# Kernel tuning notes

Hardware: AMD Instinct MI355X
Metric: run time of the kernel (lower is better)

## Reference

```python
import jax, jax.numpy as jnp
import numpy as np

N_NODES = 100000
N_EDGES = 1600000
IN_F = 256
OUT_F = 128


def setup_inputs() -> dict:
    key = jax.random.key(0)
    k1, k2, k3, k4, k5, k6 = jax.random.split(key, 6)
    init_range = float(np.sqrt(6.0 / (IN_F + OUT_F)))
    stdv = 1.0 / float(np.sqrt(OUT_F))
    return {
        "x": jax.random.normal(k1, (N_NODES, IN_F), dtype=jnp.float32),
        "weight": jax.random.uniform(k2, (IN_F, OUT_F), dtype=jnp.float32, minval=-init_range, maxval=init_range),
        "bias": jax.random.uniform(k3, (OUT_F,), dtype=jnp.float32, minval=-stdv, maxval=stdv),
        "adj_val": jax.random.uniform(k4, (N_EDGES,), dtype=jnp.float32),
        "adj_row": jax.random.randint(k5, (N_EDGES,), 0, N_NODES),  # destination node per edge
        "adj_col": jax.random.randint(k6, (N_EDGES,), 0, N_NODES),  # source node per edge
    }


def reference(x, weight, bias, adj_val, adj_row, adj_col):
    # support = X @ W   (dense GEMM, [N, in] x [in, out])
    support = x @ weight
    # output = spmm(adj, support): gather source rows, scale by edge value,
    # segment-sum into destination rows. Honors COO sparsity; no [N,N] dense.
    gathered = support[adj_col] * adj_val[:, None]          # [E, out]
    out = jax.ops.segment_sum(gathered, adj_row, num_segments=N_NODES)
    return out + bias
```

## Files before the change

kernel.cpp:

```cpp
#include <hip/hip_runtime.h>

#define N_NODES 100000
#define N_EDGES 1600000
#define IN_F 256
#define OUT_F 128
#define LDK 40

#define NBUCK 391
#define NCHUNK 256
#define CHUNK_E (N_EDGES / NCHUNK)
#define NSCAN (NBUCK * NCHUNK)
#define SCAN_BLK 4096
#define NSCAN_BLOCKS ((NSCAN + SCAN_BLK - 1) / SCAN_BLK)

#define GEMM_BM 64
#define GEMM_BLOCKS ((N_NODES + GEMM_BM - 1) / GEMM_BM)

typedef __attribute__((ext_vector_type(8))) short bf16x8;
typedef __attribute__((ext_vector_type(4))) float f32x4;

__device__ __forceinline__ unsigned short f2bf(float f) {
    unsigned u = __float_as_uint(f);
    unsigned r = u + 0x7fffu + ((u >> 16) & 1u);
    return (unsigned short)(r >> 16);
}

__global__ __launch_bounds__(256) void count_wtrans_kernel(const int* __restrict__ rowi,
                                                           int* __restrict__ counts,
                                                           const float* __restrict__ w,
                                                           unsigned short* __restrict__ wt) {
    const int tid = threadIdx.x;
    if (blockIdx.x >= NCHUNK) {
        int c = blockIdx.x - NCHUNK;
        wt[c * IN_F + tid] = f2bf(w[tid * OUT_F + c]);
        return;
    }
    __shared__ int hist[NBUCK];
    const int c = blockIdx.x;
    for (int i = tid; i < NBUCK; i += 256) hist[i] = 0;
    __syncthreads();
    const int e0 = c * CHUNK_E;
    for (int i = tid; i < CHUNK_E; i += 256)
        atomicAdd(&hist[rowi[e0 + i] >> 8], 1);
    __syncthreads();
    for (int i = tid; i < NBUCK; i += 256) counts[i * NCHUNK + c] = hist[i];
}

__global__ __launch_bounds__(256) void scan1_kernel(int* __restrict__ data,
                                                    int* __restrict__ blocksums,
                                                    int n) {
    __shared__ int sdata[256];
    const int tid = threadIdx.x;
    const int base = blockIdx.x * SCAN_BLK + tid * 16;
    int v[16];
    if (base < n) {
#pragma unroll
        for (int q = 0; q < 4; ++q) {
            int4 t = *reinterpret_cast<const int4*>(&data[base + q * 4]);
            v[q * 4 + 0] = t.x; v[q * 4 + 1] = t.y; v[q * 4 + 2] = t.z; v[q * 4 + 3] = t.w;
        }
    } else {
#pragma unroll
        for (int i = 0; i < 16; ++i) v[i] = 0;
    }
    int pre[16], run = 0;
#pragma unroll
    for (int i = 0; i < 16; ++i) { pre[i] = run; run += v[i]; }
    sdata[tid] = run;
    __syncthreads();
#pragma unroll
    for (int off = 1; off < 256; off <<= 1) {
        int t = (tid >= off) ? sdata[tid - off] : 0;
        __syncthreads();
        sdata[tid] += t;
        __syncthreads();
    }
    int excl = (tid == 0) ? 0 : sdata[tid - 1];
    if (base < n) {
#pragma unroll
        for (int q = 0; q < 4; ++q) {
            int4 t = {excl + pre[q * 4 + 0], excl + pre[q * 4 + 1],
                      excl + pre[q * 4 + 2], excl + pre[q * 4 + 3]};
            *reinterpret_cast<int4*>(&data[base + q * 4]) = t;
        }
    }
    if (tid == 255) blocksums[blockIdx.x] = sdata[255];
}

__global__ __launch_bounds__(256) void scan2_kernel(int* __restrict__ blocksums, int nblk) {
    __shared__ int sdata[256];
    const int tid = threadIdx.x;
    sdata[tid] = (tid < nblk) ? blocksums[tid] : 0;
    __syncthreads();
#pragma unroll
    for (int off = 1; off < 256; off <<= 1) {
        int t = (tid >= off) ? sdata[tid - off] : 0;
        __syncthreads();
        sdata[tid] += t;
        __syncthreads();
    }
    if (tid < nblk) blocksums[tid] = (tid == 0) ? 0 : sdata[tid - 1];
}

__global__ __launch_bounds__(256) void gemm_scatter_kernel(const float* __restrict__ x,
                                                           const unsigned short* __restrict__ wt,
                                                           unsigned short* __restrict__ support,
                                                           const int* __restrict__ rowi,
                                                           const int* __restrict__ coli,
                                                           const float* __restrict__ val,
                                                           const int* __restrict__ counts,
                                                           const int* __restrict__ blocksums,
                                                           uint2* __restrict__ tmp) {
    const int tid = threadIdx.x;

    if (blockIdx.x < NCHUNK) {
        __shared__ int cur[NBUCK];
        const int c = blockIdx.x;
        for (int i = tid; i < NBUCK; i += 256) {
            int j = i * NCHUNK + c;
            cur[i] = counts[j] + blocksums[j >> 12];
        }
        __syncthreads();
        const int e0 = c * CHUNK_E;
        for (int i = tid; i < CHUNK_E; i += 256) {
            int e = e0 + i;
            int dst = rowi[e];
            int b = dst >> 8;
            int pos = atomicAdd(&cur[b], 1);
            tmp[pos] = make_uint2(((unsigned)(dst & 255) << 17) | (unsigned)coli[e],
                                  __float_as_uint(val[e]));
        }
        return;
    }

    __shared__ unsigned short xs[GEMM_BM * LDK];
    __shared__ unsigned short ws[128 * LDK];

    const int lane = tid & 63;
    const int wv = tid >> 6;
    const int wr = (wv >> 1) * 32;
    const int wc = (wv & 1) * 64;
    const int row0 = (blockIdx.x - NCHUNK) * GEMM_BM;
    const int l15 = lane & 15;
    const int kg = (lane >> 4) * 8;

    f32x4 acc[2][4];
#pragma unroll
    for (int m = 0; m < 2; ++m)
#pragma unroll
        for (int n = 0; n < 4; ++n) acc[m][n] = (f32x4){0.f, 0.f, 0.f, 0.f};

    for (int kt = 0; kt < 8; ++kt) {
        __syncthreads();
#pragma unroll
        for (int i = 0; i < 2; ++i) {
            int idx = tid + 256 * i;
            int r = idx >> 3, q = idx & 7;
            int grow = row0 + r;
            if (grow > N_NODES - 1) grow = N_NODES - 1;
            float4 v = *reinterpret_cast<const float4*>(&x[(size_t)grow * IN_F + kt * 32 + q * 4]);
            ushort4 b;
            b.x = f2bf(v.x); b.y = f2bf(v.y); b.z = f2bf(v.z); b.w = f2bf(v.w);
            *reinterpret_cast<ushort4*>(&xs[r * LDK + q * 4]) = b;
        }
#pragma unroll
        for (int j = 0; j < 2; ++j) {
            int idx = tid + 256 * j;
            int c = idx >> 2, q = idx & 3;
            uint4 v = *reinterpret_cast<const uint4*>(&wt[c * IN_F + kt * 32 + q * 8]);
            *reinterpret_cast<uint4*>(&ws[c * LDK + q * 8]) = v;
        }
        __syncthreads();

        bf16x8 af[2], bfr[4];
#pragma unroll
        for (int m = 0; m < 2; ++m)
            af[m] = *reinterpret_cast<const bf16x8*>(&xs[(wr + m * 16 + l15) * LDK + kg]);
#pragma unroll
        for (int n = 0; n < 4; ++n)
            bfr[n] = *reinterpret_cast<const bf16x8*>(&ws[(wc + n * 16 + l15) * LDK + kg]);
#pragma unroll
        for (int m = 0; m < 2; ++m)
#pragma unroll
            for (int n = 0; n < 4; ++n)
                acc[m][n] = __builtin_amdgcn_mfma_f32_16x16x32_bf16(af[m], bfr[n], acc[m][n], 0, 0, 0);
    }

#pragma unroll
    for (int m = 0; m < 2; ++m) {
#pragma unroll
        for (int r = 0; r < 4; ++r) {
            int row = row0 + wr + m * 16 + (lane >> 4) * 4 + r;
            if (row < N_NODES) {
#pragma unroll
                for (int n = 0; n < 4; ++n) {
                    support[(size_t)row * OUT_F + wc + n * 16 + l15] = f2bf(acc[m][n][r]);
                }
            }
        }
    }
}

__global__ __launch_bounds__(256) void fine_kernel(const uint2* __restrict__ tmp,
                                                   const int* __restrict__ counts,
                                                   const int* __restrict__ blocksums,
                                                   uint2* __restrict__ pairs,
                                                   int* __restrict__ offsets) {
    __shared__ int hist[256];
    __shared__ int scanb[256];
    __shared__ int cur[256];
    const int tid = threadIdx.x, b = blockIdx.x;
    int j0 = b * NCHUNK;
    const int start = counts[j0] + blocksums[j0 >> 12];
    int end;
    if (b == NBUCK - 1) end = N_EDGES;
    else {
        int j1 = (b + 1) * NCHUNK;
        end = counts[j1] + blocksums[j1 >> 12];
    }

    hist[tid] = 0;
    __syncthreads();
    for (int i = start + tid; i < end; i += 256)
        atomicAdd(&hist[tmp[i].x >> 17], 1);
    __syncthreads();
    int h = hist[tid];
    scanb[tid] = h;
    __syncthreads();
#pragma unroll
    for (int off = 1; off < 256; off <<= 1) {
        int t = (tid >= off) ? scanb[tid - off] : 0;
        __syncthreads();
        scanb[tid] += t;
        __syncthreads();
    }
    cur[tid] = start + scanb[tid] - h;
    int node = (b << 8) + tid;
    if (node < N_NODES) offsets[node] = start + scanb[tid];
    __syncthreads();
    for (int i = start + tid; i < end; i += 256) {
        uint2 u = tmp[i];
        int dl = u.x >> 17;
        int pos = atomicAdd(&cur[dl], 1);
        pairs[pos] = make_uint2(u.x & 0x1FFFFu, u.y);
    }
}

__global__ __launch_bounds__(256) void accum_kernel(const unsigned short* __restrict__ support,
                                                    const uint2* __restrict__ pairs,
                                                    const int* __restrict__ offsets,
                                                    const float* __restrict__ bias,
                                                    float* __restrict__ out) {
    const int node = blockIdx.x * 4 + (threadIdx.x >> 6);
    const int lane = threadIdx.x & 63;
    const int grp = lane >> 4;
    const int l16 = lane & 15;
    if (node >= N_NODES) return;

    const int start = (node == 0) ? 0 : offsets[node - 1];
    const int end = offsets[node];

    float acc[8];
#pragma unroll
    for (int t = 0; t < 8; ++t) acc[t] = 0.f;

    int j = start + grp;
    for (; j + 4 < end; j += 8) {
        uint2 p0 = pairs[j];
        uint2 p1 = pairs[j + 4];
        uint4 s0 = *reinterpret_cast<const uint4*>(&support[(size_t)p0.x * OUT_F + l16 * 8]);
        uint4 s1 = *reinterpret_cast<const uint4*>(&support[(size_t)p1.x * OUT_F + l16 * 8]);
        float v0 = __uint_as_float(p0.y);
        float v1 = __uint_as_float(p1.y);
        unsigned u0[4] = {s0.x, s0.y, s0.z, s0.w};
        unsigned u1[4] = {s1.x, s1.y, s1.z, s1.w};
#pragma unroll
        for (int q = 0; q < 4; ++q) {
            acc[2 * q + 0] += __uint_as_float(u0[q] << 16) * v0;
            acc[2 * q + 1] += __uint_as_float(u0[q] & 0xffff0000u) * v0;
            acc[2 * q + 0] += __uint_as_float(u1[q] << 16) * v1;
            acc[2 * q + 1] += __uint_as_float(u1[q] & 0xffff0000u) * v1;
        }
    }
    for (; j < end; j += 4) {
        uint2 p0 = pairs[j];
        uint4 s0 = *reinterpret_cast<const uint4*>(&support[(size_t)p0.x * OUT_F + l16 * 8]);
        float v0 = __uint_as_float(p0.y);
        unsigned u0[4] = {s0.x, s0.y, s0.z, s0.w};
#pragma unroll
        for (int q = 0; q < 4; ++q) {
            acc[2 * q + 0] += __uint_as_float(u0[q] << 16) * v0;
            acc[2 * q + 1] += __uint_as_float(u0[q] & 0xffff0000u) * v0;
        }
    }

#pragma unroll
    for (int t = 0; t < 8; ++t) {
        acc[t] += __shfl_xor(acc[t], 16);
        acc[t] += __shfl_xor(acc[t], 32);
    }

    if (grp == 0) {
        float4 b0 = *reinterpret_cast<const float4*>(&bias[l16 * 8]);
        float4 b1 = *reinterpret_cast<const float4*>(&bias[l16 * 8 + 4]);
        f32x4 o0 = {acc[0] + b0.x, acc[1] + b0.y, acc[2] + b0.z, acc[3] + b0.w};
        f32x4 o1 = {acc[4] + b1.x, acc[5] + b1.y, acc[6] + b1.z, acc[7] + b1.w};
        f32x4* op = reinterpret_cast<f32x4*>(&out[(size_t)node * OUT_F + l16 * 8]);
        __builtin_nontemporal_store(o0, op);
        __builtin_nontemporal_store(o1, op + 1);
    }
}

extern "C" void kernel_launch(void* const* d_in, const int* in_sizes, int n_in,
                              void* d_out, int out_size, void* d_ws, size_t ws_size,
                              hipStream_t stream) {
    const float* x       = (const float*)d_in[0];
    const float* weight  = (const float*)d_in[1];
    const float* bias    = (const float*)d_in[2];
    const float* adj_val = (const float*)d_in[3];
    const int*   adj_row = (const int*)d_in[4];
    const int*   adj_col = (const int*)d_in[5];
    float* out = (float*)d_out;

    unsigned short* support = (unsigned short*)d_ws;
    unsigned short* wt = support + (size_t)N_NODES * OUT_F;
    int* counts = (int*)(wt + IN_F * OUT_F);
    int* blocksums = counts + NSCAN;
    int* offsets = blocksums + 32;
    uint2* tmp = (uint2*)(offsets + 100000);
    uint2* pairs = tmp + N_EDGES;

    count_wtrans_kernel<<<NCHUNK + OUT_F, 256, 0, stream>>>(adj_row, counts, weight, wt);
    scan1_kernel<<<NSCAN_BLOCKS, 256, 0, stream>>>(counts, blocksums, NSCAN);
    scan2_kernel<<<1, 256, 0, stream>>>(blocksums, NSCAN_BLOCKS);
    gemm_scatter_kernel<<<NCHUNK + GEMM_BLOCKS, 256, 0, stream>>>(
        x, wt, support, adj_row, adj_col, adj_val, counts, blocksums, tmp);
    fine_kernel<<<NBUCK, 256, 0, stream>>>(tmp, counts, blocksums, pairs, offsets);
    accum_kernel<<<(N_NODES + 3) / 4, 256, 0, stream>>>(support, pairs, offsets, bias, out);
}
```

Before: 136.7 us.

## Load GEMM tiles directly into LDS with swizzled layout, convert x to bf16 after LDS

The GEMM stage now copies x and transposed-weight tiles straight from global memory into shared memory with global_load_lds, skipping the register round trip. x is kept as fp32 in LDS and converted to bf16 only when fragments are read for MFMA. An XOR swizzle replaces the padded LDK layout to avoid bank conflicts. The trade is double the LDS footprint and read traffic for x, plus repeated conversion work per wave, and the loop still has no double buffering.

```diff
diff --git a/kernel.cpp b/kernel.cpp
--- a/kernel.cpp
+++ b/kernel.cpp
@@ -4,7 +4,6 @@
 #define N_EDGES 1600000
 #define IN_F 256
 #define OUT_F 128
-#define LDK 40
 
 #define NBUCK 391
 #define NCHUNK 256
@@ -18,6 +17,9 @@
 
 typedef __attribute__((ext_vector_type(8))) short bf16x8;
 typedef __attribute__((ext_vector_type(4))) float f32x4;
+
+typedef const __attribute__((address_space(1))) unsigned int* gas_u32;
+typedef __attribute__((address_space(3))) unsigned int* las_u32;
 
 __device__ __forceinline__ unsigned short f2bf(float f) {
     unsigned u = __float_as_uint(f);
@@ -133,8 +135,8 @@
         return;
     }
 
-    __shared__ unsigned short xs[GEMM_BM * LDK];
-    __shared__ unsigned short ws[128 * LDK];
+    __shared__ float xs[GEMM_BM * 32];
+    __shared__ unsigned short ws[128 * 32];
 
     const int lane = tid & 63;
     const int wv = tid >> 6;
@@ -142,7 +144,28 @@
     const int wc = (wv & 1) * 64;
     const int row0 = (blockIdx.x - NCHUNK) * GEMM_BM;
     const int l15 = lane & 15;
-    const int kg = (lane >> 4) * 8;
+    const int kq = lane >> 4;
+
+    const float* xg[2];
+    float* xl[2];
+#pragma unroll
+    for (int i = 0; i < 2; ++i) {
+        int idx = tid + 256 * i;
+        int r = idx >> 3, c = idx & 7;
+        int grow = row0 + r;
+        if (grow > N_NODES - 1) grow = N_NODES - 1;
+        xg[i] = &x[(size_t)grow * IN_F + ((c ^ (r & 7)) << 2)];
+        xl[i] = &xs[idx * 4];
+    }
+    const unsigned short* wg[2];
+    unsigned short* wl[2];
+#pragma unroll
+    for (int j = 0; j < 2; ++j) {
+        int idx = tid + 256 * j;
+        int col = idx >> 2, q = idx & 3;
+        wg[j] = &wt[col * IN_F + ((q ^ ((col >> 1) & 3)) << 3)];
+        wl[j] = &ws[idx * 8];
+    }
 
     f32x4 acc[2][4];
 #pragma unroll
@@ -153,32 +176,36 @@
     for (int kt = 0; kt < 8; ++kt) {
         __syncthreads();
 #pragma unroll
-        for (int i = 0; i < 2; ++i) {
-            int idx = tid + 256 * i;
-            int r = idx >> 3, q = idx & 7;
-            int grow = row0 + r;
-            if (grow > N_NODES - 1) grow = N_NODES - 1;
-            float4 v = *reinterpret_cast<const float4*>(&x[(size_t)grow * IN_F + kt * 32 + q * 4]);
-            ushort4 b;
-            b.x = f2bf(v.x); b.y = f2bf(v.y); b.z = f2bf(v.z); b.w = f2bf(v.w);
-            *reinterpret_cast<ushort4*>(&xs[r * LDK + q * 4]) = b;
-        }
-#pragma unroll
-        for (int j = 0; j < 2; ++j) {
-            int idx = tid + 256 * j;
-            int c = idx >> 2, q = idx & 3;
-            uint4 v = *reinterpret_cast<const uint4*>(&wt[c * IN_F + kt * 32 + q * 8]);
-            *reinterpret_cast<uint4*>(&ws[c * LDK + q * 8]) = v;
-        }
+        for (int i = 0; i < 2; ++i)
+            __builtin_amdgcn_global_load_lds((gas_u32)(xg[i] + kt * 32),
+                                             (las_u32)xl[i], 16, 0, 0);
+#pragma unroll
+        for (int j = 0; j < 2; ++j)
+            __builtin_amdgcn_global_load_lds((gas_u32)(wg[j] + kt * 32),
+                                             (las_u32)wl[j], 16, 0, 0);
         __syncthreads();
 
         bf16x8 af[2], bfr[4];
 #pragma unroll
-        for (int m = 0; m < 2; ++m)
-            af[m] = *reinterpret_cast<const bf16x8*>(&xs[(wr + m * 16 + l15) * LDK + kg]);
-#pragma unroll
-        for (int n = 0; n < 4; ++n)
-            bfr[n] = *reinterpret_cast<const bf16x8*>(&ws[(wc + n * 16 + l15) * LDK + kg]);
+        for (int m = 0; m < 2; ++m) {
+            int rl = wr + m * 16 + l15;
+            int s0 = (2 * kq) ^ (rl & 7);
+            int s1 = (2 * kq + 1) ^ (rl & 7);
+            f32x4 a0 = *reinterpret_cast<const f32x4*>(&xs[(rl * 8 + s0) * 4]);
+            f32x4 a1 = *reinterpret_cast<const f32x4*>(&xs[(rl * 8 + s1) * 4]);
+            bf16x8 t;
+            t[0] = (short)f2bf(a0[0]); t[1] = (short)f2bf(a0[1]);
+            t[2] = (short)f2bf(a0[2]); t[3] = (short)f2bf(a0[3]);
+            t[4] = (short)f2bf(a1[0]); t[5] = (short)f2bf(a1[1]);
+            t[6] = (short)f2bf(a1[2]); t[7] = (short)f2bf(a1[3]);
+            af[m] = t;
+        }
+#pragma unroll
+        for (int n = 0; n < 4; ++n) {
+            int cl = wc + n * 16 + l15;
+            int slot = kq ^ ((cl >> 1) & 3);
+            bfr[n] = *reinterpret_cast<const bf16x8*>(&ws[(cl * 4 + slot) * 8]);
+        }
 #pragma unroll
         for (int m = 0; m < 2; ++m)
 #pragma unroll
```

After: 132.9 us. -2.7%, faster.

## Stage full bf16 weight in swizzled LDS and load X directly into MFMA registers

Applied to the files above, without the earlier changes.

The GEMM part of the fused kernel now loads the entire 128x256 bf16 weight matrix into shared memory once per block, using an XOR swizzle to avoid bank conflicts. Each wave reads its X rows straight from global memory into registers and converts them to bf16, so the X staging buffer and the per-k-tile barriers are gone. Blocks grow to 512 threads and cover 128 rows, with each wave owning 16 rows across all 128 output columns. The price is 64KB of LDS per block, which limits how many blocks fit on a CU, and the scatter blocks now also reserve that LDS.

```diff
diff --git a/kernel.cpp b/kernel.cpp
--- a/kernel.cpp
+++ b/kernel.cpp
@@ -4,7 +4,6 @@
 #define N_EDGES 1600000
 #define IN_F 256
 #define OUT_F 128
-#define LDK 40
 
 #define NBUCK 391
 #define NCHUNK 256
@@ -13,7 +12,7 @@
 #define SCAN_BLK 4096
 #define NSCAN_BLOCKS ((NSCAN + SCAN_BLK - 1) / SCAN_BLK)
 
-#define GEMM_BM 64
+#define GEMM_BM 128
 #define GEMM_BLOCKS ((N_NODES + GEMM_BM - 1) / GEMM_BM)
 
 typedef __attribute__((ext_vector_type(8))) short bf16x8;
@@ -102,27 +101,29 @@
     if (tid < nblk) blocksums[tid] = (tid == 0) ? 0 : sdata[tid - 1];
 }
 
-__global__ __launch_bounds__(256) void gemm_scatter_kernel(const float* __restrict__ x,
-                                                           const unsigned short* __restrict__ wt,
-                                                           unsigned short* __restrict__ support,
-                                                           const int* __restrict__ rowi,
-                                                           const int* __restrict__ coli,
-                                                           const float* __restrict__ val,
-                                                           const int* __restrict__ counts,
-                                                           const int* __restrict__ blocksums,
-                                                           uint2* __restrict__ tmp) {
+__global__ __launch_bounds__(512, 4) void gemm_scatter_kernel(const float* __restrict__ x,
+                                                              const unsigned short* __restrict__ wt,
+                                                              unsigned short* __restrict__ support,
+                                                              const int* __restrict__ rowi,
+                                                              const int* __restrict__ coli,
+                                                              const float* __restrict__ val,
+                                                              const int* __restrict__ counts,
+                                                              const int* __restrict__ blocksums,
+                                                              uint2* __restrict__ tmp) {
+    __shared__ unsigned short ws[128 * 256];
+    __shared__ int cur[NBUCK];
+
     const int tid = threadIdx.x;
 
     if (blockIdx.x < NCHUNK) {
-        __shared__ int cur[NBUCK];
         const int c = blockIdx.x;
-        for (int i = tid; i < NBUCK; i += 256) {
+        for (int i = tid; i < NBUCK; i += 512) {
             int j = i * NCHUNK + c;
             cur[i] = counts[j] + blocksums[j >> 12];
         }
         __syncthreads();
         const int e0 = c * CHUNK_E;
-        for (int i = tid; i < CHUNK_E; i += 256) {
+        for (int i = tid; i < CHUNK_E; i += 512) {
             int e = e0 + i;
             int dst = rowi[e];
             int b = dst >> 8;
@@ -133,69 +134,55 @@
         return;
     }
 
-    __shared__ unsigned short xs[GEMM_BM * LDK];
-    __shared__ unsigned short ws[128 * LDK];
-
     const int lane = tid & 63;
     const int wv = tid >> 6;
-    const int wr = (wv >> 1) * 32;
-    const int wc = (wv & 1) * 64;
     const int row0 = (blockIdx.x - NCHUNK) * GEMM_BM;
     const int l15 = lane & 15;
-    const int kg = (lane >> 4) * 8;
-
-    f32x4 acc[2][4];
-#pragma unroll
-    for (int m = 0; m < 2; ++m)
-#pragma unroll
-        for (int n = 0; n < 4; ++n) acc[m][n] = (f32x4){0.f, 0.f, 0.f, 0.f};
-
+    const int kq = lane >> 4;
+
+#pragma unroll
+    for (int it = 0; it < 8; ++it) {
+        int ci = it * 512 + tid;
+        int col = ci >> 5, ch = ci & 31;
+        uint4 v = *reinterpret_cast<const uint4*>(&wt[col * IN_F + ch * 8]);
+        int slot = ch ^ (col & 7);
+        *reinterpret_cast<uint4*>(&ws[col * 256 + slot * 8]) = v;
+    }
+    __syncthreads();
+
+    int arow = row0 + wv * 16 + l15;
+    if (arow > N_NODES - 1) arow = N_NODES - 1;
+    const float* xrow = &x[(size_t)arow * IN_F + kq * 8];
+
+    f32x4 acc[8];
+#pragma unroll
+    for (int n = 0; n < 8; ++n) acc[n] = (f32x4){0.f, 0.f, 0.f, 0.f};
+
+#pragma unroll
     for (int kt = 0; kt < 8; ++kt) {
-        __syncthreads();
-#pragma unroll
-        for (int i = 0; i < 2; ++i) {
-            int idx = tid + 256 * i;
-            int r = idx >> 3, q = idx & 7;
-            int grow = row0 + r;
-            if (grow > N_NODES - 1) grow = N_NODES - 1;
-            float4 v = *reinterpret_cast<const float4*>(&x[(size_t)grow * IN_F + kt * 32 + q * 4]);
-            ushort4 b;
-            b.x = f2bf(v.x); b.y = f2bf(v.y); b.z = f2bf(v.z); b.w = f2bf(v.w);
-            *reinterpret_cast<ushort4*>(&xs[r * LDK + q * 4]) = b;
-        }
-#pragma unroll
-        for (int j = 0; j < 2; ++j) {
-            int idx = tid + 256 * j;
-            int c = idx >> 2, q = idx & 3;
-            uint4 v = *reinterpret_cast<const uint4*>(&wt[c * IN_F + kt * 32 + q * 8]);
-            *reinterpret_cast<uint4*>(&ws[c * LDK + q * 8]) = v;
-        }
-        __syncthreads();
-
-        bf16x8 af[2], bfr[4];
-#pragma unroll
-        for (int m = 0; m < 2; ++m)
-            af[m] = *reinterpret_cast<const bf16x8*>(&xs[(wr + m * 16 + l15) * LDK + kg]);
-#pragma unroll
-        for (int n = 0; n < 4; ++n)
-            bfr[n] = *reinterpret_cast<const bf16x8*>(&ws[(wc + n * 16 + l15) * LDK + kg]);
-#pragma unroll
-        for (int m = 0; m < 2; ++m)
-#pragma unroll
-            for (int n = 0; n < 4; ++n)
-                acc[m][n] = __builtin_amdgcn_mfma_f32_16x16x32_bf16(af[m], bfr[n], acc[m][n], 0, 0, 0);
-    }
-
-#pragma unroll
-    for (int m = 0; m < 2; ++m) {
-#pragma unroll
-        for (int r = 0; r < 4; ++r) {
-            int row = row0 + wr + m * 16 + (lane >> 4) * 4 + r;
-            if (row < N_NODES) {
-#pragma unroll
-                for (int n = 0; n < 4; ++n) {
-                    support[(size_t)row * OUT_F + wc + n * 16 + l15] = f2bf(acc[m][n][r]);
-                }
+        f32x4 a0 = *reinterpret_cast<const f32x4*>(xrow + kt * 32);
+        f32x4 a1 = *reinterpret_cast<const f32x4*>(xrow + kt * 32 + 4);
+        bf16x8 af;
+        af[0] = (short)f2bf(a0[0]); af[1] = (short)f2bf(a0[1]);
+        af[2] = (short)f2bf(a0[2]); af[3] = (short)f2bf(a0[3]);
+        af[4] = (short)f2bf(a1[0]); af[5] = (short)f2bf(a1[1]);
+        af[6] = (short)f2bf(a1[2]); af[7] = (short)f2bf(a1[3]);
+#pragma unroll
+        for (int n = 0; n < 8; ++n) {
+            int col = n * 16 + l15;
+            int slot = (kt * 4 + kq) ^ (col & 7);
+            bf16x8 bfv = *reinterpret_cast<const bf16x8*>(&ws[col * 256 + slot * 8]);
+            acc[n] = __builtin_amdgcn_mfma_f32_16x16x32_bf16(af, bfv, acc[n], 0, 0, 0);
+        }
+    }
+
+#pragma unroll
+    for (int r = 0; r < 4; ++r) {
+        int row = row0 + wv * 16 + kq * 4 + r;
+        if (row < N_NODES) {
+#pragma unroll
+            for (int n = 0; n < 8; ++n) {
+                support[(size_t)row * OUT_F + n * 16 + l15] = f2bf(acc[n][r]);
             }
         }
     }
@@ -333,7 +320,7 @@
     count_wtrans_kernel<<<NCHUNK + OUT_F, 256, 0, stream>>>(adj_row, counts, weight, wt);
     scan1_kernel<<<NSCAN_BLOCKS, 256, 0, stream>>>(counts, blocksums, NSCAN);
     scan2_kernel<<<1, 256, 0, stream>>>(blocksums, NSCAN_BLOCKS);
-    gemm_scatter_kernel<<<NCHUNK + GEMM_BLOCKS, 256, 0, stream>>>(
+    gemm_scatter_kernel<<<NCHUNK + GEMM_BLOCKS, 512, 0, stream>>>(
         x, wt, support, adj_row, adj_col, adj_val, counts, blocksums, tmp);
     fine_kernel<<<NBUCK, 256, 0, stream>>>(tmp, counts, blocksums, pairs, offsets);
     accum_kernel<<<(N_NODES + 3) / 4, 256, 0, stream>>>(support, pairs, offsets, bias, out);
```

New measurement: 135.3 us. No clear change (-1.0%).
